# Kernel optimization log

Hardware: AMD Instinct MI355X
Metric: run time of the kernel (lower is better)

The kernel has to match this reference:

```python
import jax, jax.numpy as jnp
import numpy as np

D_MODEL = 1024
NUM_HEADS = 16
D_K = D_MODEL // NUM_HEADS
THETA = 10000.0
MAX_SEQ_LEN = 2048
BATCH = 2
SEQ = 2048


def setup_inputs() -> dict:
    key = jax.random.key(0)
    ks = jax.random.split(key, 5)
    std = np.sqrt(2.0 / (D_MODEL + D_MODEL)).astype(np.float32)
    x = jax.random.normal(ks[0], (BATCH, SEQ, D_MODEL), dtype=jnp.float32)
    Wq = jax.random.normal(ks[1], (D_MODEL, D_MODEL), dtype=jnp.float32) * std
    Wk = jax.random.normal(ks[2], (D_MODEL, D_MODEL), dtype=jnp.float32) * std
    Wv = jax.random.normal(ks[3], (D_MODEL, D_MODEL), dtype=jnp.float32) * std
    Wo = jax.random.normal(ks[4], (D_MODEL, D_MODEL), dtype=jnp.float32) * std
    token_positions = jnp.arange(SEQ, dtype=jnp.int32)
    return {"x": x, "token_positions": token_positions,
            "Wq": Wq, "Wk": Wk, "Wv": Wv, "Wo": Wo}


def _rope_tables(positions):
    # freqs: [d_k/2]; angles: [seq, d_k/2]
    freqs = 1.0 / (THETA ** (jnp.arange(0, D_K, 2, dtype=jnp.float32) / D_K))
    angles = positions.astype(jnp.float32)[:, None] * freqs[None, :]
    return jnp.cos(angles), jnp.sin(angles)


def _apply_rope(t, cos, sin):
    # t: [b, h, s, d_k]; cos/sin: [s, d_k/2]; interleaved pair rotation
    x1 = t[..., 0::2]
    x2 = t[..., 1::2]
    r1 = x1 * cos - x2 * sin
    r2 = x1 * sin + x2 * cos
    return jnp.stack([r1, r2], axis=-1).reshape(t.shape)


def reference(x, token_positions, Wq, Wk, Wv, Wo):
    b, s, _ = x.shape
    # projections: y = x W^T
    q = jnp.einsum('bsi,oi->bso', x, Wq)
    k = jnp.einsum('bsi,oi->bso', x, Wk)
    v = jnp.einsum('bsi,oi->bso', x, Wv)
    # split heads: [b, h, s, d]
    q = q.reshape(b, s, NUM_HEADS, D_K).transpose(0, 2, 1, 3)
    k = k.reshape(b, s, NUM_HEADS, D_K).transpose(0, 2, 1, 3)
    v = v.reshape(b, s, NUM_HEADS, D_K).transpose(0, 2, 1, 3)
    cos, sin = _rope_tables(token_positions)
    q = _apply_rope(q, cos, sin)
    k = _apply_rope(k, cos, sin)
    scale = jnp.asarray(D_K, jnp.float32) ** 0.5
    scores = jnp.einsum('bhqd,bhkd->bhqk', q, k) / scale
    causal = jnp.tril(jnp.ones((s, s), dtype=bool))
    scores = jnp.where(causal, scores, -jnp.inf)
    attn = jax.nn.softmax(scores.astype(jnp.float32), axis=-1).astype(scores.dtype)
    out = jnp.einsum('bhqk,bhkd->bhqd', attn, v)
    out = out.transpose(0, 2, 1, 3).reshape(b, s, D_MODEL)
    return jnp.einsum('bsi,oi->bso', out, Wo)
```

## Files before the change

### kernel.cpp

```cpp
#include <hip/hip_runtime.h>
#include <stdint.h>

#define D_MODEL 1024
#define NH      16
#define DKH     64
#define SEQLEN  2048
#define BATCH   2
#define KDIM    1024

typedef __attribute__((ext_vector_type(8))) short          short8;
typedef __attribute__((ext_vector_type(4))) short          bf16x4;
typedef __attribute__((ext_vector_type(8))) unsigned short ushort8;
typedef __attribute__((ext_vector_type(4))) unsigned short usht4;
typedef __attribute__((ext_vector_type(4))) float          f32x4;

#define QSCALE 0.18033688011112042f

__device__ __forceinline__ unsigned short f2bf(float f) {
    union { float f; unsigned u; } v; v.f = f;
    unsigned u = v.u;
    unsigned r = (u + 0x7FFFu + ((u >> 16) & 1u)) >> 16;
    return (unsigned short)r;
}
__device__ __forceinline__ float bf2f(unsigned short h) {
    union { unsigned u; float f; } v; v.u = ((unsigned)h) << 16;
    return v.f;
}
__device__ __forceinline__ unsigned fbits(float f) {
    union { float f; unsigned u; } v; v.f = f; return v.u;
}

__device__ __forceinline__ void gload_lds16(const unsigned short* g, unsigned short* l) {
    __builtin_amdgcn_global_load_lds(
        (__attribute__((address_space(1))) void*)(g),
        (__attribute__((address_space(3))) void*)(l), 16, 0, 0);
}

__global__ void cvt_all(const float* __restrict__ X,  const float* __restrict__ Wq,
                        const float* __restrict__ Wk, const float* __restrict__ Wv,
                        const float* __restrict__ Wo,
                        unsigned short* __restrict__ Xb,  unsigned short* __restrict__ Wqb,
                        unsigned short* __restrict__ Wkb, unsigned short* __restrict__ Wvb,
                        unsigned short* __restrict__ Wob) {
    const int z = blockIdx.y;
    const float* src; unsigned short* dst; int n;
    if (z == 0)      { src = X;  dst = Xb;  n = 4194304; }
    else if (z == 1) { src = Wq; dst = Wqb; n = 1048576; }
    else if (z == 2) { src = Wk; dst = Wkb; n = 1048576; }
    else if (z == 3) { src = Wv; dst = Wvb; n = 1048576; }
    else             { src = Wo; dst = Wob; n = 1048576; }
    int i = (blockIdx.x * 256 + threadIdx.x) * 8;
    if (i >= n) return;
    float4 a = *(const float4*)(src + i);
    float4 b = *(const float4*)(src + i + 4);
    ushort8 o;
    o[0] = f2bf(a.x); o[1] = f2bf(a.y); o[2] = f2bf(a.z); o[3] = f2bf(a.w);
    o[4] = f2bf(b.x); o[5] = f2bf(b.y); o[6] = f2bf(b.z); o[7] = f2bf(b.w);
    *(ushort8*)(dst + i) = o;
}

__device__ __forceinline__ void gemm_core_128(
    const unsigned short* __restrict__ A, const unsigned short* __restrict__ W,
    unsigned short* a_lds, unsigned short* b_lds,
    int m0, int n0, f32x4 acc[4][4])
{
    const int tid  = threadIdx.x;
    const int lane = tid & 63;
    const int w    = tid >> 6;
    const int quad = lane >> 4;
    const int l16  = lane & 15;
    const int wm   = w & 1, wn = w >> 1;

    const int srow = lane >> 2;
    const int scol = (lane & 3) * 8;

    #pragma unroll
    for (int mi = 0; mi < 4; mi++)
        #pragma unroll
        for (int ni = 0; ni < 4; ni++) {
            f32x4 z = {0.f, 0.f, 0.f, 0.f};
            acc[mi][ni] = z;
        }

    for (int kk = 0; kk < KDIM; kk += 32) {
        __syncthreads();
        #pragma unroll
        for (int i = 0; i < 2; ++i) {
            int c = 2 * w + i;
            gload_lds16(A + (size_t)(m0 + c * 16 + srow) * KDIM + kk + scol, &a_lds[c * 512]);
            gload_lds16(W + (size_t)(n0 + c * 16 + srow) * KDIM + kk + scol, &b_lds[c * 512]);
        }
        __syncthreads();

        short8 af[4], bf[4];
        #pragma unroll
        for (int i = 0; i < 4; i++) {
            af[i] = *(const short8*)&a_lds[(wm * 64 + i * 16 + l16) * 32 + quad * 8];
            bf[i] = *(const short8*)&b_lds[(wn * 64 + i * 16 + l16) * 32 + quad * 8];
        }
        #pragma unroll
        for (int mi = 0; mi < 4; mi++)
            #pragma unroll
            for (int ni = 0; ni < 4; ni++)
                acc[mi][ni] = __builtin_amdgcn_mfma_f32_16x16x32_bf16(af[mi], bf[ni], acc[mi][ni], 0, 0, 0);
    }
}

__global__ __launch_bounds__(256, 2)
void gemm_qkv(const unsigned short* __restrict__ X,
              const unsigned short* __restrict__ Wq,
              const unsigned short* __restrict__ Wk,
              const unsigned short* __restrict__ Wv,
              unsigned short* __restrict__ q_ws,
              unsigned short* __restrict__ k_ws,
              unsigned short* __restrict__ v_ws)
{
    __shared__ __align__(16) unsigned short a_lds[128 * 32];
    __shared__ __align__(16) unsigned short b_lds[128 * 32];

    const int z = blockIdx.z;
    const unsigned short* W = (z == 0) ? Wq : ((z == 1) ? Wk : Wv);
    const int m0 = blockIdx.x * 128, n0 = blockIdx.y * 128;

    f32x4 acc[4][4];
    gemm_core_128(X, W, a_lds, b_lds, m0, n0, acc);

    const int lane = threadIdx.x & 63;
    const int w    = threadIdx.x >> 6;
    const int quad = lane >> 4;
    const int l16  = lane & 15;
    const int wm   = w & 1, wn = w >> 1;

    #pragma unroll
    for (int mi = 0; mi < 4; mi++)
        #pragma unroll
        for (int ni = 0; ni < 4; ni++)
            #pragma unroll
            for (int r = 0; r < 4; r++) {
                int row = m0 + wm * 64 + mi * 16 + quad * 4 + r;
                int col = n0 + wn * 64 + ni * 16 + l16;
                int b = row >> 11, s = row & 2047;
                int h = col >> 6,  d = col & 63;
                int bh = b * NH + h;
                float val = acc[mi][ni][r];
                if (z == 2) {
                    v_ws[(size_t)bh * DKH * SEQLEN + (size_t)d * SEQLEN + s] = f2bf(val);
                } else {
                    unsigned short* dst = (z == 0) ? q_ws : k_ws;
                    dst[(size_t)bh * SEQLEN * DKH + (size_t)s * DKH + d] = f2bf(val);
                }
            }
}

__global__ void rope_kernel(const int* __restrict__ pos,
                            unsigned short* __restrict__ q_ws,
                            unsigned short* __restrict__ k_ws)
{
    int i = blockIdx.x * 256 + threadIdx.x;
    int isK = i >> 19;
    unsigned short* t = isK ? k_ws : q_ws;
    float sc = isK ? 1.0f : QSCALE;
    int c   = i & 0x7FFFF;
    int bh  = c >> 14;
    int rem = c & 16383;
    int s   = rem >> 3;
    int ch  = rem & 7;
    size_t base = (size_t)bh * (SEQLEN * DKH) + (size_t)s * DKH + ch * 8;

    ushort8 v = *(ushort8*)(t + base);
    float p = (float)pos[s];
    ushort8 o;
    #pragma unroll
    for (int u = 0; u < 4; u++) {
        int j = ch * 4 + u;
        float freq = expf(-((float)(2 * j) * (1.0f / 64.0f)) * 9.210340371976184f);
        float ang = p * freq;
        float sn, cn;
        sincosf(ang, &sn, &cn);
        float x1 = bf2f(v[2 * u]);
        float x2 = bf2f(v[2 * u + 1]);
        o[2 * u]     = f2bf((x1 * cn - x2 * sn) * sc);
        o[2 * u + 1] = f2bf((x1 * sn + x2 * cn) * sc);
    }
    *(ushort8*)(t + base) = o;
}

__global__ __launch_bounds__(256, 2)
void attn_kernel(const unsigned short* __restrict__ q_ws,
                 const unsigned short* __restrict__ k_ws,
                 const unsigned short* __restrict__ v_ws,
                 unsigned short* __restrict__ ao)
{
    __shared__ __align__(16) unsigned short k_lds[128 * 72];
    __shared__ __align__(16) unsigned short v_lds[64 * 136];

    const int bh  = blockIdx.x;
    const int p   = blockIdx.y;
    const int tid = threadIdx.x, lane = tid & 63, w = tid >> 6;
    const int quad = lane >> 4, l16 = lane & 15;

    const size_t kqbase = (size_t)bh * SEQLEN * DKH;
    const size_t vbase  = (size_t)bh * DKH * SEQLEN;
    const int b = bh >> 4, h = bh & 15;

    const int krow = tid >> 3, kcol = (tid & 7) * 8;
    const int vrow = tid >> 4, vcol = (tid & 15) * 8;

    #pragma unroll
    for (int phase = 0; phase < 2; ++phase) {
        const int qt2 = (phase == 0) ? (15 - p) : p;
        const int q0  = qt2 * 128;
        const int nt  = qt2 + 1;
        const int qwbase = q0 + w * 32;

        short8 aq[2][2];
        #pragma unroll
        for (int st = 0; st < 2; st++)
            #pragma unroll
            for (int kc = 0; kc < 2; kc++)
                aq[st][kc] = *(const short8*)(q_ws + kqbase +
                    (size_t)(qwbase + st * 16 + l16) * DKH + kc * 32 + quad * 8);

        f32x4 o_acc[2][4];
        #pragma unroll
        for (int st = 0; st < 2; st++)
            #pragma unroll
            for (int df = 0; df < 4; df++) { f32x4 z = {0.f,0.f,0.f,0.f}; o_acc[st][df] = z; }
        float lsum[2] = {0.f, 0.f};

        ushort8 kreg[4], vreg[4];
        #pragma unroll
        for (int rr = 0; rr < 4; ++rr) {
            kreg[rr] = *(const ushort8*)(k_ws + kqbase + (size_t)(krow + rr * 32) * DKH + kcol);
            vreg[rr] = *(const ushort8*)(v_ws + vbase + (size_t)(vrow + rr * 16) * SEQLEN + vcol);
        }

        for (int t = 0; t < nt; ++t) {
            const int s0 = t * 128;
            __syncthreads();
            #pragma unroll
            for (int rr = 0; rr < 4; ++rr) {
                *(ushort8*)&k_lds[(krow + rr * 32) * 72 + kcol]  = kreg[rr];
                *(ushort8*)&v_lds[(vrow + rr * 16) * 136 + vcol] = vreg[rr];
            }
            __syncthreads();
            if (t < nt - 1) {
                int s1 = s0 + 128;
                #pragma unroll
                for (int rr = 0; rr < 4; ++rr) {
                    kreg[rr] = *(const ushort8*)(k_ws + kqbase + (size_t)(s1 + krow + rr * 32) * DKH + kcol);
                    vreg[rr] = *(const ushort8*)(v_ws + vbase + (size_t)(vrow + rr * 16) * SEQLEN + s1 + vcol);
                }
            }

            const bool diag = (t == nt - 1);
            #pragma unroll
            for (int nf = 0; nf < 8; nf++) {
                short8 kf0 = *(const short8*)&k_lds[(nf * 16 + l16) * 72 + 0 * 32 + quad * 8];
                short8 kf1 = *(const short8*)&k_lds[(nf * 16 + l16) * 72 + 1 * 32 + quad * 8];
                bf16x4 vf[4];
                #pragma unroll
                for (int df = 0; df < 4; df++)
                    vf[df] = *(const bf16x4*)&v_lds[(df * 16 + l16) * 136 + nf * 16 + quad * 4];

                #pragma unroll
                for (int st = 0; st < 2; st++) {
                    f32x4 s = {0.f,0.f,0.f,0.f};
                    s = __builtin_amdgcn_mfma_f32_16x16x32_bf16(kf0, aq[st][0], s, 0, 0, 0);
                    s = __builtin_amdgcn_mfma_f32_16x16x32_bf16(kf1, aq[st][1], s, 0, 0, 0);

                    if (diag) {
                        int qg = qwbase + st * 16 + l16;
                        int kg = s0 + nf * 16 + quad * 4;
                        #pragma unroll
                        for (int r = 0; r < 4; r++)
                            s[r] = (kg + r <= qg) ? __builtin_amdgcn_exp2f(s[r]) : 0.f;
                    } else {
                        #pragma unroll
                        for (int r = 0; r < 4; r++)
                            s[r] = __builtin_amdgcn_exp2f(s[r]);
                    }
                    lsum[st] += s[0] + s[1] + s[2] + s[3];

                    union { unsigned u[2]; bf16x4 v; } pk;
                    pk.u[0] = __builtin_amdgcn_perm(fbits(s[1]), fbits(s[0]), 0x07060302u);
                    pk.u[1] = __builtin_amdgcn_perm(fbits(s[3]), fbits(s[2]), 0x07060302u);

                    #pragma unroll
                    for (int df = 0; df < 4; df++)
                        o_acc[st][df] = __builtin_amdgcn_mfma_f32_16x16x16bf16_1k(vf[df], pk.v, o_acc[st][df], 0, 0, 0);
                }
            }
        }

        #pragma unroll
        for (int st = 0; st < 2; st++) {
            float rs = lsum[st];
            rs += __shfl_xor(rs, 16);
            rs += __shfl_xor(rs, 32);
            float inv = 1.0f / rs;
            int qg = qwbase + st * 16 + l16;
            #pragma unroll
            for (int df = 0; df < 4; df++) {
                usht4 ov;
                #pragma unroll
                for (int r = 0; r < 4; r++) ov[r] = f2bf(o_acc[st][df][r] * inv);
                *(usht4*)&ao[(size_t)(b * SEQLEN + qg) * D_MODEL + h * DKH + df * 16 + quad * 4] = ov;
            }
        }
    }
}

__global__ __launch_bounds__(256, 2)
void gemm_out(const unsigned short* __restrict__ AO,
              const unsigned short* __restrict__ Wo,
              float* __restrict__ out)
{
    __shared__ __align__(16) unsigned short a_lds[128 * 32];
    __shared__ __align__(16) unsigned short b_lds[128 * 32];

    const int m0 = blockIdx.x * 128, n0 = blockIdx.y * 128;
    f32x4 acc[4][4];
    gemm_core_128(AO, Wo, a_lds, b_lds, m0, n0, acc);

    const int lane = threadIdx.x & 63;
    const int w    = threadIdx.x >> 6;
    const int quad = lane >> 4;
    const int l16  = lane & 15;
    const int wm   = w & 1, wn = w >> 1;

    #pragma unroll
    for (int mi = 0; mi < 4; mi++)
        #pragma unroll
        for (int ni = 0; ni < 4; ni++)
            #pragma unroll
            for (int r = 0; r < 4; r++) {
                int row = m0 + wm * 64 + mi * 16 + quad * 4 + r;
                int col = n0 + wn * 64 + ni * 16 + l16;
                out[(size_t)row * D_MODEL + col] = acc[mi][ni][r];
            }
}

extern "C" void kernel_launch(void* const* d_in, const int* in_sizes, int n_in,
                              void* d_out, int out_size, void* d_ws, size_t ws_size,
                              hipStream_t stream) {
    const float* X  = (const float*)d_in[0];
    const int*   pos = (const int*)d_in[1];
    const float* Wq = (const float*)d_in[2];
    const float* Wk = (const float*)d_in[3];
    const float* Wv = (const float*)d_in[4];
    const float* Wo = (const float*)d_in[5];
    float* out = (float*)d_out;

    unsigned short* Xb  = (unsigned short*)d_ws;
    unsigned short* Wqb = Xb + 4194304;
    unsigned short* Wkb = Wqb + 1048576;
    unsigned short* Wvb = Wkb + 1048576;
    unsigned short* Wob = Wvb + 1048576;
    unsigned short* q_ws = Wob + 1048576;
    unsigned short* k_ws = q_ws + 4194304;
    unsigned short* v_ws = k_ws + 4194304;
    unsigned short* ao   = v_ws + 4194304;

    cvt_all<<<dim3(2048, 5), dim3(256), 0, stream>>>(X, Wq, Wk, Wv, Wo,
                                                     Xb, Wqb, Wkb, Wvb, Wob);
    gemm_qkv<<<dim3(32, 8, 3), dim3(256), 0, stream>>>(Xb, Wqb, Wkb, Wvb, q_ws, k_ws, v_ws);
    rope_kernel<<<dim3(4096), dim3(256), 0, stream>>>(pos, q_ws, k_ws);
    attn_kernel<<<dim3(32, 8), dim3(256), 0, stream>>>(q_ws, k_ws, v_ws, ao);
    gemm_out<<<dim3(32, 8), dim3(256), 0, stream>>>(ao, Wob, out);
}
```

Before: 191.2 us.

## Fuse RoPE into QKV GEMM epilogue and transpose V stores through LDS

Removes the separate rope kernel. The cos/sin table is now precomputed inside the conversion kernel as an extra grid slice, and the rotation plus Q scaling are applied in the QKV GEMM epilogue, with the pair partner fetched by a lane shuffle. The V transpose store is staged through LDS so it writes 16-byte vectorized rows instead of scattered 2-byte stores. The trade is a full extra read/write pass of Q and K against table lookups and added LDS use and syncs in the GEMM.

```diff
diff --git a/kernel.cpp b/kernel.cpp
--- a/kernel.cpp
+++ b/kernel.cpp
@@ -22,10 +22,6 @@
     unsigned r = (u + 0x7FFFu + ((u >> 16) & 1u)) >> 16;
     return (unsigned short)r;
 }
-__device__ __forceinline__ float bf2f(unsigned short h) {
-    union { unsigned u; float f; } v; v.u = ((unsigned)h) << 16;
-    return v.f;
-}
 __device__ __forceinline__ unsigned fbits(float f) {
     union { float f; unsigned u; } v; v.f = f; return v.u;
 }
@@ -38,11 +34,23 @@
 
 __global__ void cvt_all(const float* __restrict__ X,  const float* __restrict__ Wq,
                         const float* __restrict__ Wk, const float* __restrict__ Wv,
-                        const float* __restrict__ Wo,
+                        const float* __restrict__ Wo, const int* __restrict__ pos,
                         unsigned short* __restrict__ Xb,  unsigned short* __restrict__ Wqb,
                         unsigned short* __restrict__ Wkb, unsigned short* __restrict__ Wvb,
-                        unsigned short* __restrict__ Wob) {
+                        unsigned short* __restrict__ Wob, float2* __restrict__ tbl) {
     const int z = blockIdx.y;
+    if (z == 5) {
+        int i = blockIdx.x * 256 + threadIdx.x;
+        if (i < 65536) {
+            int s = i >> 5, j = i & 31;
+            float freq = expf(-((float)(2 * j) * (1.0f / 64.0f)) * 9.210340371976184f);
+            float ang = (float)pos[s] * freq;
+            float sn, cn;
+            sincosf(ang, &sn, &cn);
+            tbl[i] = make_float2(cn, sn);
+        }
+        return;
+    }
     const float* src; unsigned short* dst; int n;
     if (z == 0)      { src = X;  dst = Xb;  n = 4194304; }
     else if (z == 1) { src = Wq; dst = Wqb; n = 1048576; }
@@ -111,12 +119,14 @@
               const unsigned short* __restrict__ Wq,
               const unsigned short* __restrict__ Wk,
               const unsigned short* __restrict__ Wv,
+              const float2* __restrict__ tbl,
               unsigned short* __restrict__ q_ws,
               unsigned short* __restrict__ k_ws,
               unsigned short* __restrict__ v_ws)
 {
     __shared__ __align__(16) unsigned short a_lds[128 * 32];
     __shared__ __align__(16) unsigned short b_lds[128 * 32];
+    __shared__ __align__(16) unsigned short t_lds[32 * 136];
 
     const int z = blockIdx.z;
     const unsigned short* W = (z == 0) ? Wq : ((z == 1) ? Wk : Wv);
@@ -125,64 +135,60 @@
     f32x4 acc[4][4];
     gemm_core_128(X, W, a_lds, b_lds, m0, n0, acc);
 
-    const int lane = threadIdx.x & 63;
-    const int w    = threadIdx.x >> 6;
+    const int tid  = threadIdx.x;
+    const int lane = tid & 63;
+    const int w    = tid >> 6;
     const int quad = lane >> 4;
     const int l16  = lane & 15;
     const int wm   = w & 1, wn = w >> 1;
 
-    #pragma unroll
-    for (int mi = 0; mi < 4; mi++)
-        #pragma unroll
-        for (int ni = 0; ni < 4; ni++)
-            #pragma unroll
-            for (int r = 0; r < 4; r++) {
-                int row = m0 + wm * 64 + mi * 16 + quad * 4 + r;
-                int col = n0 + wn * 64 + ni * 16 + l16;
-                int b = row >> 11, s = row & 2047;
-                int h = col >> 6,  d = col & 63;
-                int bh = b * NH + h;
-                float val = acc[mi][ni][r];
-                if (z == 2) {
-                    v_ws[(size_t)bh * DKH * SEQLEN + (size_t)d * SEQLEN + s] = f2bf(val);
-                } else {
-                    unsigned short* dst = (z == 0) ? q_ws : k_ws;
-                    dst[(size_t)bh * SEQLEN * DKH + (size_t)s * DKH + d] = f2bf(val);
+    if (z == 2) {
+        const int bx = m0 >> 11;
+        const int c_local_w = wn * 16 + l16;
+        const int rd_c = tid >> 3;
+        const int rd_s = (tid & 7) * 16;
+        #pragma unroll
+        for (int ni = 0; ni < 4; ni++) {
+            if (ni > 0) __syncthreads();
+            #pragma unroll
+            for (int mi = 0; mi < 4; mi++) {
+                usht4 v4;
+                #pragma unroll
+                for (int r = 0; r < 4; r++) v4[r] = f2bf(acc[mi][ni][r]);
+                *(usht4*)&t_lds[c_local_w * 136 + wm * 64 + mi * 16 + quad * 4] = v4;
+            }
+            __syncthreads();
+            int col = n0 + (rd_c >> 4) * 64 + ni * 16 + (rd_c & 15);
+            int h = col >> 6, d = col & 63;
+            size_t base = (size_t)(bx * NH + h) * DKH * SEQLEN + (size_t)d * SEQLEN
+                        + (m0 & 2047) + rd_s;
+            ushort8 x0 = *(ushort8*)&t_lds[rd_c * 136 + rd_s];
+            ushort8 x1 = *(ushort8*)&t_lds[rd_c * 136 + rd_s + 8];
+            *(ushort8*)&v_ws[base]     = x0;
+            *(ushort8*)&v_ws[base + 8] = x1;
+        }
+    } else {
+        unsigned short* dst = (z == 0) ? q_ws : k_ws;
+        const float sc = (z == 0) ? QSCALE : 1.0f;
+        #pragma unroll
+        for (int mi = 0; mi < 4; mi++)
+            #pragma unroll
+            for (int ni = 0; ni < 4; ni++)
+                #pragma unroll
+                for (int r = 0; r < 4; r++) {
+                    int row = m0 + wm * 64 + mi * 16 + quad * 4 + r;
+                    int col = n0 + wn * 64 + ni * 16 + l16;
+                    int b = row >> 11, s = row & 2047;
+                    int h = col >> 6,  d = col & 63;
+                    float val = acc[mi][ni][r];
+                    float other = __shfl_xor(val, 1);
+                    float2 cs = tbl[s * 32 + (d >> 1)];
+                    float rv = (d & 1) ? (other * cs.y + val * cs.x)
+                                       : (val * cs.x - other * cs.y);
+                    dst[(size_t)(b * NH + h) * SEQLEN * DKH + (size_t)s * DKH + d] =
+                        f2bf(rv * sc);
                 }
-            }
-}
-
-__global__ void rope_kernel(const int* __restrict__ pos,
-                            unsigned short* __restrict__ q_ws,
-                            unsigned short* __restrict__ k_ws)
-{
-    int i = blockIdx.x * 256 + threadIdx.x;
-    int isK = i >> 19;
-    unsigned short* t = isK ? k_ws : q_ws;
-    float sc = isK ? 1.0f : QSCALE;
-    int c   = i & 0x7FFFF;
-    int bh  = c >> 14;
-    int rem = c & 16383;
-    int s   = rem >> 3;
-    int ch  = rem & 7;
-    size_t base = (size_t)bh * (SEQLEN * DKH) + (size_t)s * DKH + ch * 8;
-
-    ushort8 v = *(ushort8*)(t + base);
-    float p = (float)pos[s];
-    ushort8 o;
-    #pragma unroll
-    for (int u = 0; u < 4; u++) {
-        int j = ch * 4 + u;
-        float freq = expf(-((float)(2 * j) * (1.0f / 64.0f)) * 9.210340371976184f);
-        float ang = p * freq;
-        float sn, cn;
-        sincosf(ang, &sn, &cn);
-        float x1 = bf2f(v[2 * u]);
-        float x2 = bf2f(v[2 * u + 1]);
-        o[2 * u]     = f2bf((x1 * cn - x2 * sn) * sc);
-        o[2 * u + 1] = f2bf((x1 * sn + x2 * cn) * sc);
     }
-    *(ushort8*)(t + base) = o;
 }
 
 __global__ __launch_bounds__(256, 2)
@@ -361,11 +367,11 @@
     unsigned short* k_ws = q_ws + 4194304;
     unsigned short* v_ws = k_ws + 4194304;
     unsigned short* ao   = v_ws + 4194304;
-
-    cvt_all<<<dim3(2048, 5), dim3(256), 0, stream>>>(X, Wq, Wk, Wv, Wo,
-                                                     Xb, Wqb, Wkb, Wvb, Wob);
-    gemm_qkv<<<dim3(32, 8, 3), dim3(256), 0, stream>>>(Xb, Wqb, Wkb, Wvb, q_ws, k_ws, v_ws);
-    rope_kernel<<<dim3(4096), dim3(256), 0, stream>>>(pos, q_ws, k_ws);
+    float2* tbl = (float2*)(ao + 4194304);
+
+    cvt_all<<<dim3(2048, 6), dim3(256), 0, stream>>>(X, Wq, Wk, Wv, Wo, pos,
+                                                     Xb, Wqb, Wkb, Wvb, Wob, tbl);
+    gemm_qkv<<<dim3(32, 8, 3), dim3(256), 0, stream>>>(Xb, Wqb, Wkb, Wvb, tbl, q_ws, k_ws, v_ws);
     attn_kernel<<<dim3(32, 8), dim3(256), 0, stream>>>(q_ws, k_ws, v_ws, ao);
     gemm_out<<<dim3(32, 8), dim3(256), 0, stream>>>(ao, Wob, out);
 }
```

New measurement: 176.7 us. -7.6%, faster.
